# Performance work log

Hardware: AMD Instinct MI355X
Metric: run time of the kernel (lower is better)

## Reference

```python
import jax, jax.numpy as jnp
import numpy as np

N, CIN, COUT, K, CSTYLE, H, W = 8, 512, 512, 3, 512, 64, 64
EPS = 1e-8
SQRT2 = 2.0 ** 0.5


def setup_inputs() -> dict:
    key = jax.random.key(0)
    ks = jax.random.split(key, 5)
    return {
        "x": jax.random.normal(ks[0], (N, CIN, H, W), jnp.float32),
        "style": jax.random.normal(ks[1], (N, CSTYLE), jnp.float32),
        "noise": jax.random.normal(ks[2], (N, 1, H, W), jnp.float32),
        "conv_weight": jax.random.normal(ks[3], (1, COUT, CIN, K, K), jnp.float32),
        "mod_weight": jax.random.normal(ks[4], (CIN, CSTYLE), jnp.float32) / np.float32(np.sqrt(CSTYLE)),
        "mod_bias": jnp.ones((CIN,), jnp.float32),
        "noise_weight": jnp.zeros((1,), jnp.float32),
        "act_bias": jnp.zeros((COUT,), jnp.float32),
    }


def reference(x, style, noise, conv_weight, mod_weight, mod_bias, noise_weight, act_bias):
    n = x.shape[0]
    # style modulation: linear(style) -> per-sample per-in-channel scale (style_bias=0)
    s = style @ mod_weight.T + mod_bias                       # (n, cin)
    # modulate shared weight (1, cout, cin, k, k) -> (n, cout, cin, k, k)
    w = conv_weight * s[:, None, :, None, None]
    # demodulate
    demod = jax.lax.rsqrt(jnp.sum(w * w, axis=(2, 3, 4)) + EPS)  # (n, cout)
    w = w * demod[:, :, None, None, None]
    # grouped conv: groups = batch
    w = w.reshape(n * COUT, CIN, K, K)
    xg = x.reshape(1, n * CIN, H, W)
    out = jax.lax.conv_general_dilated(
        xg, w,
        window_strides=(1, 1),
        padding=[(K // 2, K // 2), (K // 2, K // 2)],
        dimension_numbers=("NCHW", "OIHW", "NCHW"),
        feature_group_count=n,
    )
    out = out.reshape(n, COUT, H, W) * SQRT2
    # noise injection (scalar weight, broadcast noise)
    out = out + noise_weight[0] * noise
    # fused bias + leaky relu (slope 0.2)
    out = jax.nn.leaky_relu(out + act_bias[None, :, None, None], negative_slope=0.2)
    return out
```

## Files before the change

### kernel.cpp

```cpp
#include <hip/hip_runtime.h>
#include <hip/hip_bf16.h>
#include <stdint.h>


typedef __attribute__((ext_vector_type(8))) short short8;
typedef __attribute__((ext_vector_type(4))) float f32x4;
typedef __attribute__((ext_vector_type(4))) unsigned int uint4v;

__device__ __forceinline__ unsigned short f2bf(float f) {
  unsigned u = __builtin_bit_cast(unsigned, f);
  u += 0x7FFFu + ((u >> 16) & 1u);
  return (unsigned short)(u >> 16);
}

__device__ __forceinline__ void g2l16(const void* g, void* l) {
  __builtin_amdgcn_global_load_lds(
      (const __attribute__((address_space(1))) void*)g,
      (__attribute__((address_space(3))) void*)l, 16, 0, 0);
}

__global__ void k_prep1(const float* __restrict__ style, const float* __restrict__ mw,
                        const float* __restrict__ mb, const float* __restrict__ cw,
                        float* __restrict__ s_out, float* __restrict__ wsq) {
  int t = threadIdx.x;
  if (blockIdx.x < 1024) {
    int wid = blockIdx.x * 4 + (t >> 6);
    int lane = t & 63;
    int n = wid >> 9, ci = wid & 511;
    float sum = 0.f;
#pragma unroll
    for (int i = 0; i < 8; ++i) {
      int k = lane + i * 64;
      sum += style[n * 512 + k] * mw[ci * 512 + k];
    }
#pragma unroll
    for (int off = 32; off; off >>= 1) sum += __shfl_xor(sum, off, 64);
    if (lane == 0) s_out[wid] = sum + mb[ci];
  } else {
    int id = (blockIdx.x - 1024) * 256 + t;
    const float* p = cw + (size_t)id * 9;
    float a = 0.f;
#pragma unroll
    for (int j = 0; j < 9; ++j) a += p[j] * p[j];
    wsq[id] = a;
  }
}

__global__ void k_demod(const float* __restrict__ s, const float* __restrict__ wsq,
                        float* __restrict__ demod) {
  int t = threadIdx.x;
  int wid = blockIdx.x * 4 + (t >> 6);
  int lane = t & 63;
  int n = wid >> 9, co = wid & 511;
  float sum = 0.f;
#pragma unroll
  for (int i = 0; i < 8; ++i) {
    int ci = lane + i * 64;
    float sv = s[n * 512 + ci];
    sum += sv * sv * wsq[co * 512 + ci];
  }
#pragma unroll
  for (int off = 32; off; off >>= 1) sum += __shfl_xor(sum, off, 64);
  if (lane == 0) demod[wid] = rsqrtf(sum + 1e-8f) * 1.41421356237309515f;
}

__global__ void k_prep3(const float* __restrict__ cw, const float* __restrict__ s,
                        const float* __restrict__ demod, const float* __restrict__ x,
                        unsigned short* __restrict__ Am, unsigned short* __restrict__ Xp) {
  __shared__ float smem[5120];
  int t = threadIdx.x;
  int b = blockIdx.x;
  if (b < 4096) {
    int n = b >> 9, co = b & 511;
    float* wrow = smem;
    float* srow = smem + 4608;
    const float* cwr = cw + (size_t)co * 4608;
#pragma unroll
    for (int i = 0; i < 18; ++i) wrow[t + i * 256] = cwr[t + i * 256];
    srow[t]       = s[n * 512 + t];
    srow[t + 256] = s[n * 512 + 256 + t];
    __syncthreads();
    float dm = demod[n * 512 + co];
    int cb = co >> 6, cr = co & 63;
    unsigned short* ob = Am + (size_t)(n * 8 + cb) * 16 * 18432 + cr * 32;
    for (int u = t; u < 576; u += 256) {
      int kb = u / 36;
      int r = u - kb * 36;
      int tap = r >> 2, q = r & 3;
      unsigned v[8];
#pragma unroll
      for (int j = 0; j < 8; ++j) {
        int ci = kb * 32 + q * 8 + j;
        v[j] = f2bf(wrow[ci * 9 + tap] * srow[ci] * dm);
      }
      uint4v o;
      o.x = v[0] | (v[1] << 16);
      o.y = v[2] | (v[3] << 16);
      o.z = v[4] | (v[5] << 16);
      o.w = v[6] | (v[7] << 16);
      *(uint4v*)(ob + (size_t)kb * 18432 + tap * 2048 + q * 8) = o;
    }
  } else {
    b -= 4096;
    int cbn = b & 7, h = (b >> 3) & 63, n = b >> 9;
    float(*lds)[65] = (float(*)[65])smem;
    const float* xb = x + (((size_t)n * 512 + cbn * 64) * 64 + h) * 64;
#pragma unroll
    for (int rep = 0; rep < 16; ++rep) {
      int idx = rep * 256 + t;
      int i = idx >> 6, w = idx & 63;
      lds[i][w] = xb[(size_t)i * 4096 + w];
    }
    __syncthreads();
    unsigned short* outb = Xp + ((size_t)(n * 66 + h + 1) * 66 + 1) * 512 + cbn * 64;
#pragma unroll
    for (int rep = 0; rep < 2; ++rep) {
      int idx = rep * 256 + t;
      int col = idx >> 3, cig = idx & 7;
      unsigned v[8];
#pragma unroll
      for (int j = 0; j < 8; ++j) v[j] = f2bf(lds[cig * 8 + j][col]);
      uint4v o;
      o.x = v[0] | (v[1] << 16);
      o.y = v[2] | (v[3] << 16);
      o.z = v[4] | (v[5] << 16);
      o.w = v[6] | (v[7] << 16);
      *(uint4v*)(outb + (size_t)col * 512 + cig * 8) = o;
    }
  }
}

__global__ void __launch_bounds__(256, 2) k_conv(
    const unsigned short* __restrict__ Am, const unsigned short* __restrict__ Xp,
    const float* __restrict__ noise, const float* __restrict__ nw_p,
    const float* __restrict__ act_bias, float* __restrict__ out) {
  __shared__ short lds_a[9 * 64 * 32];
  __shared__ short lds_x[11 * 2048];
  int t = threadIdx.x;
  int r0 = blockIdx.x * 8;
  int cb = blockIdx.y;
  int n = blockIdx.z;
  int lane = t & 63, wv = t >> 6;
  int l15 = lane & 15, lhi = lane >> 4;

  const unsigned short* abase = Am + (size_t)(n * 8 + cb) * 16 * 18432;
  const unsigned short* xbase = Xp + (size_t)n * 2230272;
  int xoffg[11];
  int t4 = t >> 2, rem = t & 3;
#pragma unroll
  for (int c = 0; c < 11; ++c) {
    int sl = c * 64 + t4;
    int rr = sl / 66, col = sl - rr * 66;
    int off = (r0 + rr) * 33792 + col * 512 + rem * 8;
    if (sl >= 660) off = 0;
    xoffg[c] = off;
  }

  f32x4 acc[4][8];
#pragma unroll
  for (int a = 0; a < 4; ++a)
#pragma unroll
    for (int b = 0; b < 8; ++b) acc[a][b] = (f32x4){0.f, 0.f, 0.f, 0.f};

  const int aoff = l15 * 32 + lhi * 8;
  const int xoff = (wv * 16 + l15) * 32 + lhi * 8;

  for (int kb = 0; kb < 16; ++kb) {
    __syncthreads();
    const char* ab = (const char*)(abase + (size_t)kb * 18432);
#pragma unroll
    for (int i = 0; i < 9; ++i)
      g2l16(ab + i * 4096 + t * 16, (char*)lds_a + i * 4096 + t * 16);
#pragma unroll
    for (int c = 0; c < 11; ++c)
      g2l16(xbase + xoffg[c] + kb * 32, (char*)lds_x + c * 4096 + t * 16);
    __syncthreads();

#pragma unroll
    for (int dw = 0; dw < 3; ++dw) {
      short8 bf[10];
#pragma unroll
      for (int rr = 0; rr < 10; ++rr)
        bf[rr] = *(const short8*)(lds_x + rr * 2112 + dw * 32 + xoff);
#pragma unroll
      for (int dh = 0; dh < 3; ++dh) {
#pragma unroll
        for (int mt = 0; mt < 4; ++mt) {
          short8 af = *(const short8*)(lds_a + ((dh * 3 + dw) * 64 + mt * 16) * 32 + aoff);
#pragma unroll
          for (int ri = 0; ri < 8; ++ri)
            acc[mt][ri] =
                __builtin_amdgcn_mfma_f32_16x16x32_bf16(af, bf[ri + dh], acc[mt][ri], 0, 0, 0);
        }
      }
    }
  }

  float nw = nw_p[0];
  int col = wv * 16 + l15;
  float nz[8];
#pragma unroll
  for (int ri = 0; ri < 8; ++ri)
    nz[ri] = nw * noise[((size_t)n * 64 + r0 + ri) * 64 + col];
#pragma unroll
  for (int mt = 0; mt < 4; ++mt) {
#pragma unroll
    for (int c = 0; c < 4; ++c) {
      int co = cb * 64 + mt * 16 + lhi * 4 + c;
      float ab2 = act_bias[co];
#pragma unroll
      for (int ri = 0; ri < 8; ++ri) {
        float v = acc[mt][ri][c] + nz[ri] + ab2;
        v = v > 0.f ? v : 0.2f * v;
        out[(((size_t)n * 512 + co) * 64 + (r0 + ri)) * 64 + col] = v;
      }
    }
  }
}

extern "C" void kernel_launch(void* const* d_in, const int* in_sizes, int n_in,
                              void* d_out, int out_size, void* d_ws, size_t ws_size,
                              hipStream_t stream) {
  const float* x     = (const float*)d_in[0];
  const float* style = (const float*)d_in[1];
  const float* noise = (const float*)d_in[2];
  const float* cw    = (const float*)d_in[3];
  const float* mw    = (const float*)d_in[4];
  const float* mb    = (const float*)d_in[5];
  const float* nw    = (const float*)d_in[6];
  const float* ab    = (const float*)d_in[7];
  float* out = (float*)d_out;

  char* ws = (char*)d_ws;
  float* s_buf  = (float*)ws;
  float* demod  = (float*)(ws + 16384);
  float* wsq    = (float*)(ws + 32768);
  unsigned short* Am = (unsigned short*)(ws + 1081344);
  unsigned short* Xp = (unsigned short*)(ws + 38830080);

  hipMemsetAsync(Xp, 0, 35684352, stream);
  k_prep1<<<2048, 256, 0, stream>>>(style, mw, mb, cw, s_buf, wsq);
  k_demod<<<1024, 256, 0, stream>>>(s_buf, wsq, demod);
  k_prep3<<<8192, 256, 0, stream>>>(cw, s_buf, demod, x, Am, Xp);
  k_conv<<<dim3(8, 8, 8), 256, 0, stream>>>(Am, Xp, noise, nw, ab, out);
}
```

Baseline: 285.5 us.

## Move style modulation onto activations and demod into epilogue, share one weight tensor

Instead of building a per-sample modulated bf16 weight tensor (8x the weights), the style scale is applied to the input activations while they are converted to bf16. The demodulation factor is applied to the accumulator in the conv epilogue, so a single shared bf16 weight tensor serves all samples. The weight and activation layouts are reorganized into MFMA fragment order, and the demod pass is merged into the activation-prep kernel, removing one launch. This cuts prep work and weight memory traffic, but rounding to bf16 now happens after scaling activations rather than weights, which changes numerics slightly.

```diff
diff --git a/kernel.cpp b/kernel.cpp
--- a/kernel.cpp
+++ b/kernel.cpp
@@ -21,10 +21,13 @@
 
 __global__ void k_prep1(const float* __restrict__ style, const float* __restrict__ mw,
                         const float* __restrict__ mb, const float* __restrict__ cw,
-                        float* __restrict__ s_out, float* __restrict__ wsq) {
+                        float* __restrict__ s_out, float* __restrict__ wsq,
+                        unsigned short* __restrict__ Wt) {
+  __shared__ float ldsf[18432];
   int t = threadIdx.x;
-  if (blockIdx.x < 1024) {
-    int wid = blockIdx.x * 4 + (t >> 6);
+  int b = blockIdx.x;
+  if (b < 1024) {
+    int wid = b * 4 + (t >> 6);
     int lane = t & 63;
     int n = wid >> 9, ci = wid & 511;
     float sum = 0.f;
@@ -36,73 +39,67 @@
 #pragma unroll
     for (int off = 32; off; off >>= 1) sum += __shfl_xor(sum, off, 64);
     if (lane == 0) s_out[wid] = sum + mb[ci];
-  } else {
-    int id = (blockIdx.x - 1024) * 256 + t;
+  } else if (b < 2048) {
+    int id = (b - 1024) * 256 + t;
     const float* p = cw + (size_t)id * 9;
     float a = 0.f;
 #pragma unroll
     for (int j = 0; j < 9; ++j) a += p[j] * p[j];
     wsq[id] = a;
-  }
-}
-
-__global__ void k_demod(const float* __restrict__ s, const float* __restrict__ wsq,
-                        float* __restrict__ demod) {
-  int t = threadIdx.x;
-  int wid = blockIdx.x * 4 + (t >> 6);
-  int lane = t & 63;
-  int n = wid >> 9, co = wid & 511;
-  float sum = 0.f;
-#pragma unroll
-  for (int i = 0; i < 8; ++i) {
-    int ci = lane + i * 64;
-    float sv = s[n * 512 + ci];
-    sum += sv * sv * wsq[co * 512 + ci];
-  }
-#pragma unroll
-  for (int off = 32; off; off >>= 1) sum += __shfl_xor(sum, off, 64);
-  if (lane == 0) demod[wid] = rsqrtf(sum + 1e-8f) * 1.41421356237309515f;
-}
-
-__global__ void k_prep3(const float* __restrict__ cw, const float* __restrict__ s,
-                        const float* __restrict__ demod, const float* __restrict__ x,
-                        unsigned short* __restrict__ Am, unsigned short* __restrict__ Xp) {
-  __shared__ float smem[5120];
-  int t = threadIdx.x;
-  int b = blockIdx.x;
-  if (b < 4096) {
-    int n = b >> 9, co = b & 511;
-    float* wrow = smem;
-    float* srow = smem + 4608;
-    const float* cwr = cw + (size_t)co * 4608;
-#pragma unroll
-    for (int i = 0; i < 18; ++i) wrow[t + i * 256] = cwr[t + i * 256];
-    srow[t]       = s[n * 512 + t];
-    srow[t + 256] = s[n * 512 + 256 + t];
-    __syncthreads();
-    float dm = demod[n * 512 + co];
-    int cb = co >> 6, cr = co & 63;
-    unsigned short* ob = Am + (size_t)(n * 8 + cb) * 16 * 18432 + cr * 32;
-    for (int u = t; u < 576; u += 256) {
-      int kb = u / 36;
-      int r = u - kb * 36;
-      int tap = r >> 2, q = r & 3;
+  } else {
+    int bb = b - 2048;
+    int cb = bb >> 4, kb = bb & 15;
+#pragma unroll
+    for (int i = 0; i < 72; ++i) {
+      int idx = t + i * 256;
+      int seg = idx / 288, off = idx - seg * 288;
+      ldsf[idx] = cw[(size_t)(cb * 64 + seg) * 4608 + kb * 288 + off];
+    }
+    __syncthreads();
+    unsigned short* ob = Wt + (size_t)(cb * 16 + kb) * 18432;
+#pragma unroll
+    for (int i = 0; i < 9; ++i) {
+      int c = t + i * 256;
+      int m = c & 15, lhi = (c >> 4) & 3, mt = (c >> 6) & 3, tap = c >> 8;
+      int co_rel = mt * 16 + m;
       unsigned v[8];
 #pragma unroll
-      for (int j = 0; j < 8; ++j) {
-        int ci = kb * 32 + q * 8 + j;
-        v[j] = f2bf(wrow[ci * 9 + tap] * srow[ci] * dm);
-      }
+      for (int j = 0; j < 8; ++j)
+        v[j] = f2bf(ldsf[co_rel * 288 + (lhi * 8 + j) * 9 + tap]);
       uint4v o;
       o.x = v[0] | (v[1] << 16);
       o.y = v[2] | (v[3] << 16);
       o.z = v[4] | (v[5] << 16);
       o.w = v[6] | (v[7] << 16);
-      *(uint4v*)(ob + (size_t)kb * 18432 + tap * 2048 + q * 8) = o;
-    }
+      *(uint4v*)(ob + (size_t)c * 8) = o;
+    }
+  }
+}
+
+__global__ void k_prep2(const float* __restrict__ s, const float* __restrict__ wsq,
+                        const float* __restrict__ x, float* __restrict__ demod,
+                        unsigned short* __restrict__ Xp) {
+  __shared__ float smem[4225];
+  __shared__ float sx[64];
+  int t = threadIdx.x;
+  int b = blockIdx.x;
+  if (b < 1024) {
+    int wid = b * 4 + (t >> 6);
+    int lane = t & 63;
+    int n = wid >> 9, co = wid & 511;
+    float sum = 0.f;
+#pragma unroll
+    for (int i = 0; i < 8; ++i) {
+      int ci = lane + i * 64;
+      float sv = s[n * 512 + ci];
+      sum += sv * sv * wsq[co * 512 + ci];
+    }
+#pragma unroll
+    for (int off = 32; off; off >>= 1) sum += __shfl_xor(sum, off, 64);
+    if (lane == 0) demod[wid] = rsqrtf(sum + 1e-8f) * 1.41421356237309515f;
   } else {
-    b -= 4096;
-    int cbn = b & 7, h = (b >> 3) & 63, n = b >> 9;
+    int b2 = b - 1024;
+    int cbn = b2 & 7, h = (b2 >> 3) & 63, n = b2 >> 9;
     float(*lds)[65] = (float(*)[65])smem;
     const float* xb = x + (((size_t)n * 512 + cbn * 64) * 64 + h) * 64;
 #pragma unroll
@@ -111,31 +108,34 @@
       int i = idx >> 6, w = idx & 63;
       lds[i][w] = xb[(size_t)i * 4096 + w];
     }
-    __syncthreads();
-    unsigned short* outb = Xp + ((size_t)(n * 66 + h + 1) * 66 + 1) * 512 + cbn * 64;
+    if (t < 64) sx[t] = s[n * 512 + cbn * 64 + t];
+    __syncthreads();
+    unsigned short* nb = Xp + (size_t)n * 2230272 + (size_t)(h + 1) * 33792;
 #pragma unroll
     for (int rep = 0; rep < 2; ++rep) {
-      int idx = rep * 256 + t;
-      int col = idx >> 3, cig = idx & 7;
+      int c = rep * 256 + t;
+      int cig = c >> 6, col = c & 63;
+      int kb = cbn * 2 + (cig >> 2), lhi = cig & 3;
       unsigned v[8];
 #pragma unroll
-      for (int j = 0; j < 8; ++j) v[j] = f2bf(lds[cig * 8 + j][col]);
+      for (int j = 0; j < 8; ++j) v[j] = f2bf(lds[cig * 8 + j][col] * sx[cig * 8 + j]);
       uint4v o;
       o.x = v[0] | (v[1] << 16);
       o.y = v[2] | (v[3] << 16);
       o.z = v[4] | (v[5] << 16);
       o.w = v[6] | (v[7] << 16);
-      *(uint4v*)(outb + (size_t)col * 512 + cig * 8) = o;
+      *(uint4v*)(nb + ((size_t)(kb * 4 + lhi) * 66 + col + 1) * 8) = o;
     }
   }
 }
 
 __global__ void __launch_bounds__(256, 2) k_conv(
-    const unsigned short* __restrict__ Am, const unsigned short* __restrict__ Xp,
-    const float* __restrict__ noise, const float* __restrict__ nw_p,
-    const float* __restrict__ act_bias, float* __restrict__ out) {
-  __shared__ short lds_a[9 * 64 * 32];
-  __shared__ short lds_x[11 * 2048];
+    const unsigned short* __restrict__ Wt, const unsigned short* __restrict__ Xp,
+    const float* __restrict__ demod, const float* __restrict__ noise,
+    const float* __restrict__ nw_p, const float* __restrict__ act_bias,
+    float* __restrict__ out) {
+  __shared__ short lds_a[18432];
+  __shared__ short lds_x[22528];
   int t = threadIdx.x;
   int r0 = blockIdx.x * 8;
   int cb = blockIdx.y;
@@ -143,27 +143,26 @@
   int lane = t & 63, wv = t >> 6;
   int l15 = lane & 15, lhi = lane >> 4;
 
-  const unsigned short* abase = Am + (size_t)(n * 8 + cb) * 16 * 18432;
+  const unsigned short* abase = Wt + (size_t)cb * 16 * 18432;
   const unsigned short* xbase = Xp + (size_t)n * 2230272;
   int xoffg[11];
-  int t4 = t >> 2, rem = t & 3;
-#pragma unroll
-  for (int c = 0; c < 11; ++c) {
-    int sl = c * 64 + t4;
-    int rr = sl / 66, col = sl - rr * 66;
-    int off = (r0 + rr) * 33792 + col * 512 + rem * 8;
-    if (sl >= 660) off = 0;
-    xoffg[c] = off;
+#pragma unroll
+  for (int j = 0; j < 11; ++j) {
+    int c = j * 256 + t;
+    int r = c / 264, rc = c - r * 264;
+    int off = (r0 + r) * 33792 + rc * 8;
+    if (c >= 2640) off = 0;
+    xoffg[j] = off;
   }
 
   f32x4 acc[4][8];
 #pragma unroll
   for (int a = 0; a < 4; ++a)
 #pragma unroll
-    for (int b = 0; b < 8; ++b) acc[a][b] = (f32x4){0.f, 0.f, 0.f, 0.f};
-
-  const int aoff = l15 * 32 + lhi * 8;
-  const int xoff = (wv * 16 + l15) * 32 + lhi * 8;
+    for (int bq = 0; bq < 8; ++bq) acc[a][bq] = (f32x4){0.f, 0.f, 0.f, 0.f};
+
+  const int aoff = lhi * 128 + l15 * 8;
+  const int xoffb = lhi * 528 + (wv * 16 + l15) * 8;
 
   for (int kb = 0; kb < 16; ++kb) {
     __syncthreads();
@@ -172,8 +171,8 @@
     for (int i = 0; i < 9; ++i)
       g2l16(ab + i * 4096 + t * 16, (char*)lds_a + i * 4096 + t * 16);
 #pragma unroll
-    for (int c = 0; c < 11; ++c)
-      g2l16(xbase + xoffg[c] + kb * 32, (char*)lds_x + c * 4096 + t * 16);
+    for (int j = 0; j < 11; ++j)
+      g2l16(xbase + xoffg[j] + kb * 2112, (char*)lds_x + j * 4096 + t * 16);
     __syncthreads();
 
 #pragma unroll
@@ -181,12 +180,12 @@
       short8 bf[10];
 #pragma unroll
       for (int rr = 0; rr < 10; ++rr)
-        bf[rr] = *(const short8*)(lds_x + rr * 2112 + dw * 32 + xoff);
+        bf[rr] = *(const short8*)(lds_x + rr * 2112 + dw * 8 + xoffb);
 #pragma unroll
       for (int dh = 0; dh < 3; ++dh) {
 #pragma unroll
         for (int mt = 0; mt < 4; ++mt) {
-          short8 af = *(const short8*)(lds_a + ((dh * 3 + dw) * 64 + mt * 16) * 32 + aoff);
+          short8 af = *(const short8*)(lds_a + (dh * 3 + dw) * 2048 + mt * 512 + aoff);
 #pragma unroll
           for (int ri = 0; ri < 8; ++ri)
             acc[mt][ri] =
@@ -204,13 +203,15 @@
     nz[ri] = nw * noise[((size_t)n * 64 + r0 + ri) * 64 + col];
 #pragma unroll
   for (int mt = 0; mt < 4; ++mt) {
+    f32x4 dm4 = *(const f32x4*)(demod + n * 512 + cb * 64 + mt * 16 + lhi * 4);
 #pragma unroll
     for (int c = 0; c < 4; ++c) {
       int co = cb * 64 + mt * 16 + lhi * 4 + c;
       float ab2 = act_bias[co];
+      float dm = dm4[c];
 #pragma unroll
       for (int ri = 0; ri < 8; ++ri) {
-        float v = acc[mt][ri][c] + nz[ri] + ab2;
+        float v = dm * acc[mt][ri][c] + nz[ri] + ab2;
         v = v > 0.f ? v : 0.2f * v;
         out[(((size_t)n * 512 + co) * 64 + (r0 + ri)) * 64 + col] = v;
       }
@@ -235,12 +236,11 @@
   float* s_buf  = (float*)ws;
   float* demod  = (float*)(ws + 16384);
   float* wsq    = (float*)(ws + 32768);
-  unsigned short* Am = (unsigned short*)(ws + 1081344);
-  unsigned short* Xp = (unsigned short*)(ws + 38830080);
+  unsigned short* Wt = (unsigned short*)(ws + 1081344);
+  unsigned short* Xp = (unsigned short*)(ws + 5799936);
 
   hipMemsetAsync(Xp, 0, 35684352, stream);
-  k_prep1<<<2048, 256, 0, stream>>>(style, mw, mb, cw, s_buf, wsq);
-  k_demod<<<1024, 256, 0, stream>>>(s_buf, wsq, demod);
-  k_prep3<<<8192, 256, 0, stream>>>(cw, s_buf, demod, x, Am, Xp);
-  k_conv<<<dim3(8, 8, 8), 256, 0, stream>>>(Am, Xp, noise, nw, ab, out);
-}
+  k_prep1<<<2176, 256, 0, stream>>>(style, mw, mb, cw, s_buf, wsq, Wt);
+  k_prep2<<<5120, 256, 0, stream>>>(s_buf, wsq, x, demod, Xp);
+  k_conv<<<dim3(8, 8, 8), 256, 0, stream>>>(Wt, Xp, demod, noise, nw, ab, out);
+}
```

Measured after the change: 280.0 us. No clear change (-1.9%).
